# Kernel tuning notes

Measured on AMD Instinct MI355X. Metric: run time of the kernel, lower is better.

## Reference

```python
import jax, jax.numpy as jnp
import numpy as np

H_IMG = W_IMG = 1024
H_MAP = W_MAP = 64
SCALE = 16  # img // fmap, both axes
SCALES = [2, 2.5, 3, 3.5, 4, 5]
RATIOS = [0.5, 1.5, 2.0, 2.5, 3, 3.5, 4]
A = len(SCALES) * len(RATIOS)  # 42
POS_T, NEG_T = 0.5, 0.3


def _anchors_np():
    # generate_base_anchors + generate_anchor_boxes (down_h = down_w = SCALE)
    base = np.zeros((A, 4), np.float32)
    cy = cx = SCALE / 2.0
    i = 0
    for s in SCALES:
        for ar in RATIOS:
            h = SCALE * s * np.sqrt(ar)
            w = SCALE * s * np.sqrt(1.0 / ar)
            base[i] = [cy - h / 2.0, cx - w / 2.0, cy + h / 2.0, cx + w / 2.0]
            i += 1
    sy = np.arange(H_MAP) * SCALE
    sx = np.arange(W_MAP) * SCALE
    gx, gy = np.meshgrid(sx, sy)
    shifts = np.stack([gy.ravel(), gx.ravel(), gy.ravel(), gx.ravel()], axis=1)
    # order (H, W, A) -> matches conf.permute(0,2,3,1) flatten
    return (base[None, :, :] + shifts[:, None, :]).reshape(-1, 4).astype(np.float32)


def _conv(x, w, b):
    y = jax.lax.conv_general_dilated(x, w, (1, 1), 'SAME',
                                     dimension_numbers=('NCHW', 'OIHW', 'NCHW'))
    return y + b[None, :, None, None]


def setup_inputs() -> dict:
    key = jax.random.key(0)
    ks = jax.random.split(key, 10)
    B, N, C, Hm, Wm, HID = 8, 20, 256, 64, 64, 512
    feature_map = jax.random.normal(ks[0], (B, C, Hm, Wm), dtype=jnp.float32)
    # valid GT boxes in pixel xyxy-style (d0<d2, d1<d3), last 5 per image padded -1
    p0 = jax.random.uniform(ks[1], (B, N)) * 860.0
    p1 = jax.random.uniform(ks[2], (B, N)) * 860.0
    s0 = jax.random.uniform(ks[3], (B, N)) * 144.0 + 16.0
    s1 = jax.random.uniform(ks[4], (B, N)) * 144.0 + 16.0
    gt_bboxes = jnp.stack([p0, p1, p0 + s0, p1 + s1], axis=-1)
    gt_bboxes = gt_bboxes.at[:, 15:, :].set(-1.0)
    gt_classes = jax.random.randint(ks[5], (B, N), 0, 10)
    conv1_w = jax.random.normal(ks[6], (HID, C, 3, 3), dtype=jnp.float32) * 0.02
    conv1_b = jnp.zeros((HID,), jnp.float32)
    conf_w = jax.random.normal(ks[7], (A, HID, 1, 1), dtype=jnp.float32) * 0.02
    conf_b = jnp.zeros((A,), jnp.float32)
    reg_w = jax.random.normal(ks[8], (4 * A, HID, 1, 1), dtype=jnp.float32) * 0.02
    reg_b = jnp.zeros((4 * A,), jnp.float32)
    return {"feature_map": feature_map, "gt_bboxes": gt_bboxes, "gt_classes": gt_classes,
            "conv1_w": conv1_w, "conv1_b": conv1_b, "conf_w": conf_w, "conf_b": conf_b,
            "reg_w": reg_w, "reg_b": reg_b}


def reference(feature_map, gt_bboxes, gt_classes, conv1_w, conv1_b,
              conf_w, conf_b, reg_w, reg_b):
    anc = jnp.asarray(_anchors_np())           # [M,4]
    B = feature_map.shape[0]
    M = anc.shape[0]                           # H*W*A

    # project_bboxes p2a: divide by scale, keep -1 padding
    pad = gt_bboxes == -1.0
    g = jnp.where(pad, -1.0, gt_bboxes / float(SCALE))  # [B,N,4]
    valid = g[..., 0] >= 0                                # [B,N]
    g_safe = jnp.where(valid[..., None], g, jnp.array([0.0, 0.0, 1.0, 1.0]))

    # pairwise IoU [B,M,N] (vectorized get_iou_mat; invalid GT -> 0)
    tl = jnp.maximum(anc[None, :, None, :2], g_safe[:, None, :, :2])
    br = jnp.minimum(anc[None, :, None, 2:], g_safe[:, None, :, 2:])
    wh = jnp.clip(br - tl, 0.0)
    inter = wh[..., 0] * wh[..., 1]
    area_a = (anc[:, 2] - anc[:, 0]) * (anc[:, 3] - anc[:, 1])
    area_g = (g_safe[..., 2] - g_safe[..., 0]) * (g_safe[..., 3] - g_safe[..., 1])
    iou = inter / (area_a[None, :, None] + area_g[:, None, :] - inter)
    iou = jnp.where(valid[:, None, :], iou, 0.0)

    # positive assignment: per-GT argmax anchors + IoU > pos_thresh
    max_per_gt = iou.max(axis=1, keepdims=True)            # [B,1,N]
    pos_mask = ((iou == max_per_gt) & (max_per_gt > 0)) | (iou > POS_T)
    pos_any = pos_mask.any(axis=-1)                        # [B,M]
    a2g = jnp.argmax(iou, axis=2)                          # [B,M]
    max_per_anc = iou.max(axis=2)                          # [B,M]

    gt_for_anc = jnp.take_along_axis(g_safe, a2g[:, :, None], axis=1)  # [B,M,4]
    anc_b = jnp.broadcast_to(anc, (B, M, 4))
    gt_sel = jnp.where(pos_any[..., None], gt_for_anc, anc_b)  # safe for log

    # calc_gt_offsets (cxcywh encode), computed for all anchors, masked later
    a_c = (anc_b[..., :2] + anc_b[..., 2:]) * 0.5
    a_s = anc_b[..., 2:] - anc_b[..., :2]
    g_c = (gt_sel[..., :2] + gt_sel[..., 2:]) * 0.5
    g_s = gt_sel[..., 2:] - gt_sel[..., :2]
    off_gt = jnp.concatenate([(g_c - a_c) / a_s, jnp.log(g_s / a_s)], axis=-1)
    off_gt = off_gt.reshape(-1, 4)                          # [B*M,4]

    # ProposalModule head (dropout is a no-op in eval)
    x = jax.nn.relu(_conv(feature_map, conv1_w, conv1_b))
    conf = _conv(x, conf_w, conf_b)                         # [B,A,H,W]
    reg = _conv(x, reg_w, reg_b)                            # [B,4A,H,W]
    cflat = conf.transpose(0, 2, 3, 1).reshape(-1)          # [B*M]
    offp = reg.transpose(0, 2, 3, 1).reshape(-1, 4)         # [B*M,4]

    pf = pos_any.reshape(-1).astype(jnp.float32)
    P = pf.sum()

    # cls loss: BCE-with-logits, label 1 on positives, 0 on P sampled negatives
    cls_pos = (jax.nn.softplus(-cflat) * pf).sum() / P
    neg = max_per_anc.reshape(-1) < NEG_T
    scores = jax.random.uniform(jax.random.key(7), cflat.shape)
    scores = jnp.where(neg, scores, 2.0)
    ranks = jnp.argsort(jnp.argsort(scores))               # random sample = rank < P
    sel = (neg & (ranks < P)).astype(jnp.float32)
    cls_neg = (jax.nn.softplus(cflat) * sel).sum() / sel.sum()
    cls_loss = 0.5 * (cls_pos + cls_neg)

    d = offp - off_gt
    ad = jnp.abs(d)
    sl1 = jnp.where(ad < 1.0, 0.5 * ad * ad, ad - 0.5)
    reg_loss = (sl1 * pf[:, None]).sum() / (P * 4.0)

    return cls_loss + reg_loss
```

## Files before the change

kernel.cpp:

```cpp
#include <hip/hip_runtime.h>
#include <hip/hip_fp16.h>
#include <stdint.h>

constexpr int B_  = 8, HM = 64, WM = 64, A_ = 42, CIN = 256, HIDN = 512;
constexpr int M_  = HM * WM * A_;
constexpr int NA  = B_ * M_;
constexpr int HALF = NA / 2;
constexpr int KK  = CIN * 9;
constexpr float POS_T = 0.5f;

constexpr int WINY = 10, WINX = 10, WPIX = WINY * WINX;
constexpr int PERIMG = A_ * WPIX;
constexpr int WBLK = (PERIMG + 511) / 512;
constexpr int NMAXB = WBLK * B_;

constexpr int MAXPOS = 4096, MAXSEL = 4096, MAXCAND = 16384, MAXTIE = 256;
constexpr int MAXPIX = 1024;
constexpr uint32_t VCAND = 16384u;

constexpr int KSPL = 8, KCH = KK / KSPL;
constexpr int NSTRIP = MAXPIX / 64;
constexpr int NOCH = 4;
constexpr int NTILE = NSTRIP * NOCH * KSPL;
constexpr int TFBLK = HALF / 512;
constexpr int WCVTB = (HIDN * KK / 4) / 512;
constexpr int NBLK_TF = NMAXB + TFBLK + WCVTB;

constexpr size_t OFF_CTRL  = 0;
constexpr size_t OFF_BINS  = 256;
constexpr size_t OFF_MAXGT = 768;
constexpr size_t OFF_SLOT  = 2048;
constexpr size_t MS_END    = 133120;
constexpr size_t OFF_PLIST = 133120;
constexpr size_t OFF_POSL  = 137216;
constexpr size_t OFF_SELL  = 153600;
constexpr size_t OFF_CAND  = 169984;
constexpr size_t OFF_PART  = 301056;
constexpr size_t OFF_APATCH= 8689664;
constexpr size_t OFF_WF16  = 13408256;
constexpr size_t OFF_HFIN  = 15767552;


__device__ __forceinline__ unsigned short f2bf(float f) {
  uint32_t x = __float_as_uint(f);
  uint32_t r = x + 0x7FFFu + ((x >> 16) & 1u);
  return (unsigned short)(r >> 16);
}
__device__ __forceinline__ float bf2f(unsigned short h) {
  return __uint_as_float(((uint32_t)h) << 16);
}
__device__ __forceinline__ uint32_t f2h2(float a, float b) {
  return (uint32_t)__half_as_ushort(__float2half_rn(a)) |
         ((uint32_t)__half_as_ushort(__float2half_rn(b)) << 16);
}

typedef _Float16 h8v __attribute__((ext_vector_type(8)));
typedef float f4v __attribute__((ext_vector_type(4)));

__device__ __forceinline__ float iou_pair(float ay0, float ax0, float ay1, float ax1,
                                          float areaA, float g0, float g1, float g2, float g3,
                                          float areaG) {
#pragma clang fp contract(off)
  float ty = fmaxf(ay0, g0), tx = fmaxf(ax0, g1);
  float by = fminf(ay1, g2), bx = fminf(ax1, g3);
  float hy = by - ty; hy = fmaxf(hy, 0.f);
  float hx = bx - tx; hx = fmaxf(hx, 0.f);
  float inter = hy * hx;
  return inter / (areaA + areaG - inter);
}

__device__ __forceinline__ void anchor_box(const float* basef, int a, int y, int x,
                                           float& ay0, float& ax0, float& ay1, float& ax1,
                                           float& areaA) {
#pragma clang fp contract(off)
  double sy = 16.0 * (double)y, sx = 16.0 * (double)x;
  ay0 = (float)((double)basef[a * 4 + 0] + sy);
  ax0 = (float)((double)basef[a * 4 + 1] + sx);
  ay1 = (float)((double)basef[a * 4 + 2] + sy);
  ax1 = (float)((double)basef[a * 4 + 3] + sx);
  areaA = (ay1 - ay0) * (ax1 - ax0);
}

__device__ __forceinline__ void fill_base(float* sbase, int t) {
  if (t < 42) {
    const double SC[6] = {2.0, 2.5, 3.0, 3.5, 4.0, 5.0};
    const double RA[7] = {0.5, 1.5, 2.0, 2.5, 3.0, 3.5, 4.0};
    int si = t / 7, ri = t - si * 7;
    double h = 16.0 * SC[si] * sqrt(RA[ri]);
    double w = 16.0 * SC[si] * sqrt(1.0 / RA[ri]);
    sbase[t * 4 + 0] = (float)(8.0 - h / 2.0);
    sbase[t * 4 + 1] = (float)(8.0 - w / 2.0);
    sbase[t * 4 + 2] = (float)(8.0 + h / 2.0);
    sbase[t * 4 + 3] = (float)(8.0 + w / 2.0);
  }
}

__device__ __forceinline__ void fill_gt(const float* gt, int b, float* sg, float* sarea,
                                        unsigned* sval, int t) {
  if (t < 20) {
#pragma clang fp contract(off)
    float g4[4];
    for (int d = 0; d < 4; d++) {
      float v = gt[(b * 20 + t) * 4 + d];
      g4[d] = (v == -1.0f) ? -1.0f : v * 0.0625f;
    }
    unsigned valid = (g4[0] >= 0.0f) ? 1u : 0u;
    if (!valid) { g4[0] = 0.f; g4[1] = 0.f; g4[2] = 1.f; g4[3] = 1.f; }
    sg[t * 4 + 0] = g4[0]; sg[t * 4 + 1] = g4[1]; sg[t * 4 + 2] = g4[2]; sg[t * 4 + 3] = g4[3];
    sarea[t] = (g4[2] - g4[0]) * (g4[3] - g4[1]);
    sval[t] = valid;
  }
}

__device__ __forceinline__ void claim_pixel(char* ws, int pixg) {
  int* slotmap = (int*)(ws + OFF_SLOT);
  if (atomicCAS((unsigned*)&slotmap[pixg], 0u, 0xFFFFFFFFu) == 0u) {
    unsigned s = atomicAdd((unsigned*)(ws + OFF_CTRL) + 2, 1u);
    if (s < MAXPIX) { ((int*)(ws + OFF_PLIST))[s] = pixg; slotmap[pixg] = (int)s + 1; }
    else slotmap[pixg] = -1;
  }
}

__device__ __forceinline__ float softplusf(float x) {
  return fmaxf(x, 0.f) + log1pf(expf(-fabsf(x)));
}
__device__ __forceinline__ float sl1(float d) {
  float ad = fabsf(d);
  return ad < 1.f ? 0.5f * ad * ad : ad - 0.5f;
}

__device__ __forceinline__ void tf_round(uint32_t& x0, uint32_t& x1, int r) {
  x0 += x1; x1 = (x1 << r) | (x1 >> (32 - r)); x1 ^= x0;
}
__device__ __forceinline__ void threefry(uint32_t c0, uint32_t c1, uint32_t& o0, uint32_t& o1) {
  const uint32_t k0 = 0u, k1 = 7u;
  const uint32_t k2 = k0 ^ k1 ^ 0x1BD11BDAu;
  uint32_t x0 = c0 + k0, x1 = c1 + k1;
  tf_round(x0, x1, 13); tf_round(x0, x1, 15); tf_round(x0, x1, 26); tf_round(x0, x1, 6);
  x0 += k1; x1 += k2 + 1u;
  tf_round(x0, x1, 17); tf_round(x0, x1, 29); tf_round(x0, x1, 16); tf_round(x0, x1, 24);
  x0 += k2; x1 += k0 + 2u;
  tf_round(x0, x1, 13); tf_round(x0, x1, 15); tf_round(x0, x1, 26); tf_round(x0, x1, 6);
  x0 += k0; x1 += k1 + 3u;
  tf_round(x0, x1, 17); tf_round(x0, x1, 29); tf_round(x0, x1, 16); tf_round(x0, x1, 24);
  x0 += k1; x1 += k2 + 4u;
  tf_round(x0, x1, 13); tf_round(x0, x1, 15); tf_round(x0, x1, 26); tf_round(x0, x1, 6);
  x0 += k2; x1 += k0 + 5u;
  o0 = x0; o1 = x1;
}

__device__ __forceinline__ void dev_threefry_emit(char* ws, int p, int lane) {
  uint32_t o0, o1; threefry((uint32_t)p, (uint32_t)(p + HALF), o0, o1);
  uint32_t v0 = o0 >> 9, v1 = o1 >> 9;
  unsigned* ctrl = (unsigned*)(ws + OFF_CTRL);
  unsigned* bins = (unsigned*)(ws + OFF_BINS);
  uint2* cand = (uint2*)(ws + OFF_CAND);
  bool h0 = v0 < VCAND, h1 = v1 < VCAND;
  unsigned long long m0 = __ballot(h0), m1 = __ballot(h1);
  if (m0 | m1) {
    int n0 = __popcll(m0);
    int leader = (int)__ffsll(m0 | m1) - 1;
    unsigned base = 0;
    if (lane == leader) base = atomicAdd(&ctrl[3], (unsigned)(n0 + __popcll(m1)));
    base = (unsigned)__shfl((int)base, leader, 64);
    unsigned long long below = (1ull << lane) - 1ull;
    if (h0) {
      unsigned s = base + (unsigned)__popcll(m0 & below);
      if (s < MAXCAND) cand[s] = make_uint2(v0, (unsigned)p);
      atomicAdd(&bins[v0 >> 7], 1u);
    }
    if (h1) {
      unsigned s = base + (unsigned)n0 + (unsigned)__popcll(m1 & below);
      if (s < MAXCAND) cand[s] = make_uint2(v1, (unsigned)(p + HALF));
      atomicAdd(&bins[v1 >> 7], 1u);
    }
  }
}

__global__ void __launch_bounds__(512) kTF(const float* __restrict__ gt,
                                           const float* __restrict__ w1, char* ws) {
  __shared__ float sbase[168], sg[80], sarea[20];
  __shared__ unsigned sval[20];
  __shared__ int smax[20];
  int t = threadIdx.x, lane = t & 63;
  if (blockIdx.x < NMAXB) {
    int b = blockIdx.x / WBLK, blk = blockIdx.x - b * WBLK;
    fill_base(sbase, t);
    fill_gt(gt, b, sg, sarea, sval, t);
    if (t < 20) smax[t] = 0;
    __syncthreads();
    int idx = blk * 512 + t;
    bool ok = idx < PERIMG;
    float ay0 = 0.f, ax0 = 0.f, ay1 = 0.f, ax1 = 0.f, areaA = 1.f;
    if (ok) {
      int a = idx / WPIX, pp = idx - a * WPIX;
      int y = pp / WINX, x = pp - y * WINX;
      anchor_box(sbase, a, y, x, ay0, ax0, ay1, ax1, areaA);
    }
#pragma unroll
    for (int n = 0; n < 20; n++) {
      float io = 0.f;
      if (ok && sval[n]) io = iou_pair(ay0, ax0, ay1, ax1, areaA,
                                       sg[n * 4], sg[n * 4 + 1], sg[n * 4 + 2],
                                       sg[n * 4 + 3], sarea[n]);
#pragma unroll
      for (int off = 32; off >= 1; off >>= 1) io = fmaxf(io, __shfl_xor(io, off, 64));
      if ((t & 63) == 0 && io > 0.f) atomicMax(&smax[n], __float_as_int(io));
    }
    __syncthreads();
    if (t < 20 && smax[t] != 0)
      atomicMax((int*)(ws + OFF_MAXGT) + b * 20 + t, smax[t]);
  } else if (blockIdx.x < NMAXB + TFBLK) {
    int p = ((int)blockIdx.x - NMAXB) * 512 + t;
    if (p < HALF) dev_threefry_emit(ws, p, lane);
  } else {
    int q = ((int)blockIdx.x - (NMAXB + TFBLK)) * 512 + t;
    float4 v = ((const float4*)w1)[q];
    uint2 o;
    o.x = f2h2(v.x, v.y);
    o.y = f2h2(v.z, v.w);
    ((uint2*)(ws + OFF_WF16))[q] = o;
  }
}

__global__ void __launch_bounds__(512) kPos2(const float* __restrict__ gt, char* ws) {
  __shared__ float sbase[168], sg[80], sarea[20], smg[20];
  __shared__ unsigned sval[20];
  int b = blockIdx.y, t = threadIdx.x;
  unsigned* ctrl = (unsigned*)(ws + OFF_CTRL);
  fill_base(sbase, t);
  fill_gt(gt, b, sg, sarea, sval, t);
  if (t < 20) smg[t] = __int_as_float(((int*)(ws + OFF_MAXGT))[b * 20 + t]);
  __syncthreads();
  int idx = blockIdx.x * 512 + t;
  bool pos = false;
  unsigned packv = 0;
  int pixg = 0;
  if (idx < PERIMG) {
    int a = idx / WPIX, pp = idx - a * WPIX;
    int y = pp / WINX, x = pp - y * WINX;
    float ay0, ax0, ay1, ax1, areaA;
    anchor_box(sbase, a, y, x, ay0, ax0, ay1, ax1, areaA);
    float best = -1.f; int arg = 0;
#pragma unroll
    for (int n = 0; n < 20; n++) {
      float io = 0.f;
      if (sval[n]) io = iou_pair(ay0, ax0, ay1, ax1, areaA,
                                 sg[n * 4], sg[n * 4 + 1], sg[n * 4 + 2],
                                 sg[n * 4 + 3], sarea[n]);
      if (io > best) { best = io; arg = n; }
      float mg = smg[n];
      pos = pos || ((io == mg) && (mg > 0.f)) || (io > POS_T);
    }
    if (pos) {
      int pix = y * 64 + x;
      int i = b * M_ + pix * 42 + a;
      packv = (unsigned)i | ((unsigned)arg << 21);
      pixg = b * 4096 + pix;
    }
  }
  unsigned long long mask = __ballot(pos);
  if (mask) {
    int lane = t & 63;
    int leader = (int)__ffsll(mask) - 1;
    unsigned base = 0;
    if (lane == leader) base = atomicAdd(&ctrl[0], (unsigned)__popcll(mask));
    base = (unsigned)__shfl((int)base, leader, 64);
    if (pos) {
      unsigned slot = base + (unsigned)__popcll(mask & ((1ull << lane) - 1ull));
      if (slot < MAXPOS) ((unsigned*)(ws + OFF_POSL))[slot] = packv;
      claim_pixel(ws, pixg);
    }
  }
}

__global__ void __launch_bounds__(1024) kSel(char* ws) {
  __shared__ unsigned selbins[128];
  __shared__ uint2 ties[MAXTIE];
  __shared__ unsigned tcnt, s_r, s_ucut;
  __shared__ int s_icut, s_cutbin;
  int t = threadIdx.x;
  unsigned* ctrl = (unsigned*)(ws + OFF_CTRL);
  const uint2* cand = (const uint2*)(ws + OFF_CAND);
  unsigned P = min(ctrl[0], (unsigned)MAXPOS);
  unsigned nc = min(ctrl[3], (unsigned)MAXCAND);
  if (t < 128) selbins[t] = ((const unsigned*)(ws + OFF_BINS))[t];
  if (t == 0) tcnt = 0;
  __syncthreads();
  if (t == 0) {
    unsigned cum = 0; int c = 0;
    for (; c < 128; c++) { if (cum + selbins[c] >= P) break; cum += selbins[c]; }
    if (c == 128) c = 127;
    s_cutbin = c; s_r = (P > cum) ? (P - cum) : 0u;
  }
  __syncthreads();
  int cutbin = s_cutbin;
  for (unsigned j = t; j < nc; j += 1024) {
    uint2 cj = cand[j];
    if ((int)(cj.x >> 7) == cutbin) {
      unsigned k = atomicAdd(&tcnt, 1u);
      if (k < MAXTIE) ties[k] = cj;
    }
  }
  __syncthreads();
  unsigned n = min(tcnt, (unsigned)MAXTIE);
  unsigned r = s_r; if (r > n) r = n;
  if (r == 0) {
    if (t == 0) { s_ucut = 0; s_icut = -1; }
  } else if (t < (int)n) {
    uint2 mine = ties[t];
    unsigned rank = 0;
    for (unsigned j = 0; j < n; j++) {
      uint2 o = ties[j];
      if (o.x < mine.x || (o.x == mine.x && (int)o.y < (int)mine.y)) rank++;
    }
    if (rank == r - 1) { s_ucut = mine.x; s_icut = (int)mine.y; }
  }
  __syncthreads();
  unsigned ucut = s_ucut; int icut = s_icut;
  unsigned total = (nc + 1023u) & ~1023u;
  for (unsigned j = t; j < total; j += 1024) {
    bool sel = false; uint2 cj = make_uint2(0u, 0u);
    if (j < nc) {
      cj = cand[j];
      sel = (cj.x < ucut) || (cj.x == ucut && (int)cj.y <= icut);
    }
    unsigned long long mask = __ballot(sel);
    if (mask) {
      int lane = t & 63;
      int leader = (int)__ffsll(mask) - 1;
      unsigned base = 0;
      if (lane == leader) base = atomicAdd(&ctrl[1], (unsigned)__popcll(mask));
      base = (unsigned)__shfl((int)base, leader, 64);
      if (sel) {
        unsigned slot = base + (unsigned)__popcll(mask & ((1ull << lane) - 1ull));
        if (slot < MAXSEL) {
          ((int*)(ws + OFF_SELL))[slot] = (int)cj.y;
          int bb = (int)cj.y / M_; int m = (int)cj.y - bb * M_;
          claim_pixel(ws, bb * 4096 + m / 42);
        }
      }
    }
  }
}

__global__ void __launch_bounds__(256) kIm2col(const float* __restrict__ fm, char* ws) {
  unsigned* ctrl = (unsigned*)(ws + OFF_CTRL);
  int npix = min((int)ctrl[2], MAXPIX);
  int blk = blockIdx.x;
  if (blk >= npix) return;
  int chunk = blockIdx.y;
  int pixg = ((const int*)(ws + OFF_PLIST))[blk];
  int b = pixg >> 12, pix = pixg & 4095;
  int y = pix >> 6, x = pix & 63;
  uint32_t* Ap = (uint32_t*)(ws + OFF_APATCH) + (size_t)blk * (KK / 2);
  int u0 = chunk * 384;
  for (int u = u0 + threadIdx.x; u < u0 + 384; u += 256) {
    float v[2];
#pragma unroll
    for (int h = 0; h < 2; h++) {
      int k = 2 * u + h;
      int ic = k / 9, r = k - ic * 9;
      int dy = r / 3, dx = r - dy * 3;
      int yy = y + dy - 1, xx = x + dx - 1;
      float vv = 0.f;
      if (yy >= 0 && yy < 64 && xx >= 0 && xx < 64)
        vv = fm[(((size_t)b * CIN + ic) * 64 + yy) * 64 + xx];
      v[h] = vv;
    }
    Ap[u] = f2h2(v[0], v[1]);
  }
}

__global__ void __launch_bounds__(256) kGemm(char* ws) {
  unsigned* ctrl = (unsigned*)(ws + OFF_CTRL);
  int npix = min((int)ctrl[2], MAXPIX);
  int tile = blockIdx.x;
  int strip = tile & 15, r2 = tile >> 4;
  int och = r2 & 3, ks = r2 >> 2;
  int px0 = strip * 64;
  if (px0 >= npix) return;
  int oc0 = och * 128, kb = ks * KCH;
  const _Float16* Ap = (const _Float16*)(ws + OFF_APATCH);
  const _Float16* Wf = (const _Float16*)(ws + OFF_WF16);
  int t = threadIdx.x, lane = t & 63, wv = t >> 6;
  int kq = lane >> 4;
  const _Float16* Arow = Ap + (size_t)(px0 + wv * 16 + (lane & 15)) * KK + kb + kq * 8;
  const _Float16* Wrow = Wf + (size_t)(oc0 + (lane & 15)) * KK + kb + kq * 8;
  f4v acc[8] = {};
#pragma unroll 3
  for (int s = 0; s < 9; s++) {
    h8v a = *(const h8v*)(Arow + s * 32);
#pragma unroll
    for (int o = 0; o < 8; o++) {
      h8v bfr = *(const h8v*)(Wrow + (size_t)o * 16 * KK + s * 32);
      acc[o] = __builtin_amdgcn_mfma_f32_16x16x32_f16(a, bfr, acc[o], 0, 0, 0);
    }
  }
  unsigned short* part = (unsigned short*)(ws + OFF_PART) + (size_t)ks * MAXPIX * HIDN;
  int colbase = oc0 + (lane & 15);
  int pxb = px0 + wv * 16 + kq * 4;
#pragma unroll
  for (int o = 0; o < 8; o++) {
#pragma unroll
    for (int r = 0; r < 4; r++) {
      int px = pxb + r;
      if (px < npix)
        part[(size_t)px * HIDN + colbase + o * 16] = f2bf(acc[o][r]);
    }
  }
}

__global__ void __launch_bounds__(256) kReduce(const float* __restrict__ b1, char* ws) {
  unsigned* ctrl = (unsigned*)(ws + OFF_CTRL);
  int npix = min((int)ctrl[2], MAXPIX);
  int px = blockIdx.x;
  if (px >= npix) return;
  int t = threadIdx.x;
  constexpr size_t PS = (size_t)MAXPIX * HIDN;
  const unsigned short* p0 = (const unsigned short*)(ws + OFF_PART);
  unsigned short* hf = (unsigned short*)(ws + OFF_HFIN);
  size_t off = (size_t)px * HIDN + t * 2;
  float s0 = b1[t * 2], s1 = b1[t * 2 + 1];
#pragma unroll
  for (int q = 0; q < KSPL; q++) {
    uint32_t v = *(const uint32_t*)(p0 + q * PS + off);
    s0 += bf2f((unsigned short)(v & 0xFFFFu));
    s1 += bf2f((unsigned short)(v >> 16));
  }
  s0 = fmaxf(s0, 0.f); s1 = fmaxf(s1, 0.f);
  *(uint32_t*)(hf + off) = f2h2(s0, s1);
}

__global__ void __launch_bounds__(256) kHead(const float* __restrict__ gt,
                                             const float* __restrict__ cw,
                                             const float* __restrict__ cb,
                                             const float* __restrict__ rw,
                                             const float* __restrict__ rb,
                                             char* ws, float* out) {
  __shared__ float sbase[168], sg[640];
  __shared__ float sacc[3];
  int t = threadIdx.x;
  fill_base(sbase, t);
  if (t < 160) {
#pragma clang fp contract(off)
    float g4[4];
    for (int d = 0; d < 4; d++) {
      float v = gt[t * 4 + d];
      g4[d] = (v == -1.0f) ? -1.0f : v * 0.0625f;
    }
    if (!(g4[0] >= 0.0f)) { g4[0] = 0.f; g4[1] = 0.f; g4[2] = 1.f; g4[3] = 1.f; }
    sg[t * 4 + 0] = g4[0]; sg[t * 4 + 1] = g4[1];
    sg[t * 4 + 2] = g4[2]; sg[t * 4 + 3] = g4[3];
  }
  if (t < 3) sacc[t] = 0.f;
  __syncthreads();
  unsigned* ctrl = (unsigned*)(ws + OFF_CTRL);
  float* accum = (float*)(ctrl + 16);
  int np = min((int)ctrl[0], MAXPOS);
  int ns = min((int)ctrl[1], MAXSEL);
  int nent = np + ns;
  const unsigned* posl = (const unsigned*)(ws + OFF_POSL);
  const int* sell = (const int*)(ws + OFF_SELL);
  const int* slotmap = (const int*)(ws + OFF_SLOT);
  const unsigned short* hfin = (const unsigned short*)(ws + OFF_HFIN);
  int lane = t & 63;
  int gwave = blockIdx.x * 4 + (t >> 6);
  int nwaves = gridDim.x * 4;
  for (int e = gwave; e < nent; e += nwaves) {
    bool isPos = e < np;
    int i, arg = 0;
    if (isPos) { unsigned pck = posl[e]; i = (int)(pck & 0x1FFFFFu); arg = (int)(pck >> 21); }
    else i = sell[e - np];
    int b = i / M_; int m = i - b * M_;
    int pix = m / 42; int a = m - pix * 42;
    int y = pix >> 6, x = pix & 63;
    int slot = slotmap[b * 4096 + pix] - 1;
    if (slot < 0 || slot >= MAXPIX) continue;
    float h[8];
    {
      h8v hv = *(const h8v*)(hfin + (size_t)slot * HIDN + lane * 8);
#pragma unroll
      for (int j = 0; j < 8; j++) h[j] = (float)hv[j];
    }
    const float* cwr = cw + (size_t)a * HIDN + lane * 8;
    float4 cA = *(const float4*)cwr;
    float4 cB = *(const float4*)(cwr + 4);
    float cp = h[0] * cA.x + h[1] * cA.y + h[2] * cA.z + h[3] * cA.w +
               h[4] * cB.x + h[5] * cB.y + h[6] * cB.z + h[7] * cB.w;
#pragma unroll
    for (int off = 32; off >= 1; off >>= 1) cp += __shfl_xor(cp, off, 64);
    float conf = cp + cb[a];
    if (isPos) {
      float rp[4];
#pragma unroll
      for (int d = 0; d < 4; d++) {
        const float* rwr = rw + (size_t)(a * 4 + d) * HIDN + lane * 8;
        float4 rA = *(const float4*)rwr;
        float4 rB = *(const float4*)(rwr + 4);
        float sd = h[0] * rA.x + h[1] * rA.y + h[2] * rA.z + h[3] * rA.w +
                   h[4] * rB.x + h[5] * rB.y + h[6] * rB.z + h[7] * rB.w;
#pragma unroll
        for (int off = 32; off >= 1; off >>= 1) sd += __shfl_xor(sd, off, 64);
        rp[d] = sd + rb[a * 4 + d];
      }
      if (lane == 0) {
#pragma clang fp contract(off)
        float ay0, ax0, ay1, ax1, areaA;
        anchor_box(sbase, a, y, x, ay0, ax0, ay1, ax1, areaA);
        const float* g = sg + (size_t)(b * 20 + arg) * 4;
        float acy = (ay0 + ay1) * 0.5f, acx = (ax0 + ax1) * 0.5f;
        float ah = ay1 - ay0, aw = ax1 - ax0;
        float gcy = (g[0] + g[2]) * 0.5f, gcx = (g[1] + g[3]) * 0.5f;
        float gh = g[2] - g[0], gw = g[3] - g[1];
        float t0 = (gcy - acy) / ah, t1 = (gcx - acx) / aw;
        float t2 = logf(gh / ah), t3 = logf(gw / aw);
        float sL = sl1(rp[0] - t0) + sl1(rp[1] - t1) + sl1(rp[2] - t2) + sl1(rp[3] - t3);
        atomicAdd(&sacc[2], sL);
        atomicAdd(&sacc[0], softplusf(-conf));
      }
    } else {
      if (lane == 0) atomicAdd(&sacc[1], softplusf(conf));
    }
  }
  __syncthreads();
  if (t == 0) {
    if (sacc[0] != 0.f) atomicAdd(&accum[0], sacc[0]);
    if (sacc[1] != 0.f) atomicAdd(&accum[1], sacc[1]);
    if (sacc[2] != 0.f) atomicAdd(&accum[2], sacc[2]);
    __threadfence();
    unsigned done = atomicAdd(&ctrl[10], 1u);
    if (done == gridDim.x - 1) {
      __threadfence();
      float P = (float)min((int)ctrl[0], MAXPOS);
      float S = (float)min((int)ctrl[1], MAXSEL);
      float cls = 0.5f * (accum[0] / P + accum[1] / S);
      out[0] = cls + accum[2] / (P * 4.0f);
    }
  }
}

extern "C" void kernel_launch(void* const* d_in, const int* in_sizes, int n_in,
                              void* d_out, int out_size, void* d_ws, size_t ws_size,
                              hipStream_t stream) {
  const float* fm = (const float*)d_in[0];
  const float* gt = (const float*)d_in[1];
  const float* w1 = (const float*)d_in[3];
  const float* b1 = (const float*)d_in[4];
  const float* cw = (const float*)d_in[5];
  const float* cb = (const float*)d_in[6];
  const float* rw = (const float*)d_in[7];
  const float* rb = (const float*)d_in[8];
  char* ws = (char*)d_ws;
  float* out = (float*)d_out;

  hipMemsetAsync(ws, 0, MS_END, stream);
  kTF<<<NBLK_TF, 512, 0, stream>>>(gt, w1, ws);
  kPos2<<<dim3(WBLK, B_), 512, 0, stream>>>(gt, ws);
  kSel<<<1, 1024, 0, stream>>>(ws);
  kIm2col<<<dim3(MAXPIX, 3), 256, 0, stream>>>(fm, ws);
  kGemm<<<NTILE, 256, 0, stream>>>(ws);
  kReduce<<<MAXPIX, 256, 0, stream>>>(b1, ws);
  kHead<<<256, 256, 0, stream>>>(gt, cw, cb, rw, rb, ws, out);
}
```

Baseline: 177.8 us.

## Fold selection into last kPos2 block and fuse split-K reduce into GEMM

The separate single-block kSel kernel is removed. Its work now runs in the last kPos2 block to finish, detected with an atomic ticket counter, which saves one launch. The GEMM changes from a split-K grid that wrote bf16 partials to global memory plus a separate kReduce kernel. Now each block handles 16 pixels and its 8 waves split K, reducing through shared memory with bias, ReLU and fp16 store fused in. This drops the partial-sum round trip and a launch, but gives fewer pixels per block and adds relaxed-atomic completion logic in kHead.

```diff
diff --git a/kernel.cpp b/kernel.cpp
--- a/kernel.cpp
+++ b/kernel.cpp
@@ -18,10 +18,7 @@
 constexpr int MAXPIX = 1024;
 constexpr uint32_t VCAND = 16384u;
 
-constexpr int KSPL = 8, KCH = KK / KSPL;
-constexpr int NSTRIP = MAXPIX / 64;
-constexpr int NOCH = 4;
-constexpr int NTILE = NSTRIP * NOCH * KSPL;
+constexpr int KCH = 288;
 constexpr int TFBLK = HALF / 512;
 constexpr int WCVTB = (HIDN * KK / 4) / 512;
 constexpr int NBLK_TF = NMAXB + TFBLK + WCVTB;
@@ -35,7 +32,6 @@
 constexpr size_t OFF_POSL  = 137216;
 constexpr size_t OFF_SELL  = 153600;
 constexpr size_t OFF_CAND  = 169984;
-constexpr size_t OFF_PART  = 301056;
 constexpr size_t OFF_APATCH= 8689664;
 constexpr size_t OFF_WF16  = 13408256;
 constexpr size_t OFF_HFIN  = 15767552;
@@ -226,7 +222,11 @@
 __global__ void __launch_bounds__(512) kPos2(const float* __restrict__ gt, char* ws) {
   __shared__ float sbase[168], sg[80], sarea[20], smg[20];
   __shared__ unsigned sval[20];
-  int b = blockIdx.y, t = threadIdx.x;
+  __shared__ unsigned selbins[128];
+  __shared__ uint2 ties[MAXTIE];
+  __shared__ unsigned tcnt, s_r, s_ucut;
+  __shared__ int s_icut, s_cutbin, s_last;
+  int b = blockIdx.y, t = threadIdx.x, lane = t & 63;
   unsigned* ctrl = (unsigned*)(ws + OFF_CTRL);
   fill_base(sbase, t);
   fill_gt(gt, b, sg, sarea, sval, t);
@@ -261,7 +261,6 @@
   }
   unsigned long long mask = __ballot(pos);
   if (mask) {
-    int lane = t & 63;
     int leader = (int)__ffsll(mask) - 1;
     unsigned base = 0;
     if (lane == leader) base = atomicAdd(&ctrl[0], (unsigned)__popcll(mask));
@@ -272,18 +271,19 @@
       claim_pixel(ws, pixg);
     }
   }
-}
-
-__global__ void __launch_bounds__(1024) kSel(char* ws) {
-  __shared__ unsigned selbins[128];
-  __shared__ uint2 ties[MAXTIE];
-  __shared__ unsigned tcnt, s_r, s_ucut;
-  __shared__ int s_icut, s_cutbin;
-  int t = threadIdx.x;
-  unsigned* ctrl = (unsigned*)(ws + OFF_CTRL);
+  __syncthreads();
+  if (t == 0) {
+    unsigned r = __hip_atomic_fetch_add(&ctrl[11], 1u, __ATOMIC_RELAXED,
+                                        __HIP_MEMORY_SCOPE_AGENT);
+    s_last = (r == (unsigned)(WBLK * B_) - 1) ? 1 : 0;
+  }
+  __syncthreads();
+  if (!s_last) return;
   const uint2* cand = (const uint2*)(ws + OFF_CAND);
-  unsigned P = min(ctrl[0], (unsigned)MAXPOS);
-  unsigned nc = min(ctrl[3], (unsigned)MAXCAND);
+  unsigned P = min(__hip_atomic_load(&ctrl[0], __ATOMIC_RELAXED,
+                                     __HIP_MEMORY_SCOPE_AGENT), (unsigned)MAXPOS);
+  unsigned nc = min(__hip_atomic_load(&ctrl[3], __ATOMIC_RELAXED,
+                                      __HIP_MEMORY_SCOPE_AGENT), (unsigned)MAXCAND);
   if (t < 128) selbins[t] = ((const unsigned*)(ws + OFF_BINS))[t];
   if (t == 0) tcnt = 0;
   __syncthreads();
@@ -295,7 +295,7 @@
   }
   __syncthreads();
   int cutbin = s_cutbin;
-  for (unsigned j = t; j < nc; j += 1024) {
+  for (unsigned j = t; j < nc; j += 512) {
     uint2 cj = cand[j];
     if ((int)(cj.x >> 7) == cutbin) {
       unsigned k = atomicAdd(&tcnt, 1u);
@@ -318,22 +318,21 @@
   }
   __syncthreads();
   unsigned ucut = s_ucut; int icut = s_icut;
-  unsigned total = (nc + 1023u) & ~1023u;
-  for (unsigned j = t; j < total; j += 1024) {
+  unsigned total = (nc + 511u) & ~511u;
+  for (unsigned j = t; j < total; j += 512) {
     bool sel = false; uint2 cj = make_uint2(0u, 0u);
     if (j < nc) {
       cj = cand[j];
       sel = (cj.x < ucut) || (cj.x == ucut && (int)cj.y <= icut);
     }
-    unsigned long long mask = __ballot(sel);
-    if (mask) {
-      int lane = t & 63;
-      int leader = (int)__ffsll(mask) - 1;
+    unsigned long long m2 = __ballot(sel);
+    if (m2) {
+      int leader = (int)__ffsll(m2) - 1;
       unsigned base = 0;
-      if (lane == leader) base = atomicAdd(&ctrl[1], (unsigned)__popcll(mask));
+      if (lane == leader) base = atomicAdd(&ctrl[1], (unsigned)__popcll(m2));
       base = (unsigned)__shfl((int)base, leader, 64);
       if (sel) {
-        unsigned slot = base + (unsigned)__popcll(mask & ((1ull << lane) - 1ull));
+        unsigned slot = base + (unsigned)__popcll(m2 & ((1ull << lane) - 1ull));
         if (slot < MAXSEL) {
           ((int*)(ws + OFF_SELL))[slot] = (int)cj.y;
           int bb = (int)cj.y / M_; int m = (int)cj.y - bb * M_;
@@ -372,20 +371,20 @@
   }
 }
 
-__global__ void __launch_bounds__(256) kGemm(char* ws) {
+__global__ void __launch_bounds__(512) kGemm(const float* __restrict__ b1, char* ws) {
+  __shared__ float red[8][16][132];
   unsigned* ctrl = (unsigned*)(ws + OFF_CTRL);
   int npix = min((int)ctrl[2], MAXPIX);
-  int tile = blockIdx.x;
-  int strip = tile & 15, r2 = tile >> 4;
-  int och = r2 & 3, ks = r2 >> 2;
-  int px0 = strip * 64;
+  int strip = blockIdx.x, och = blockIdx.y;
+  int px0 = strip * 16;
   if (px0 >= npix) return;
-  int oc0 = och * 128, kb = ks * KCH;
+  int oc0 = och * 128;
   const _Float16* Ap = (const _Float16*)(ws + OFF_APATCH);
   const _Float16* Wf = (const _Float16*)(ws + OFF_WF16);
   int t = threadIdx.x, lane = t & 63, wv = t >> 6;
   int kq = lane >> 4;
-  const _Float16* Arow = Ap + (size_t)(px0 + wv * 16 + (lane & 15)) * KK + kb + kq * 8;
+  int kb = wv * KCH;
+  const _Float16* Arow = Ap + (size_t)(px0 + (lane & 15)) * KK + kb + kq * 8;
   const _Float16* Wrow = Wf + (size_t)(oc0 + (lane & 15)) * KK + kb + kq * 8;
   f4v acc[8] = {};
 #pragma unroll 3
@@ -397,39 +396,31 @@
       acc[o] = __builtin_amdgcn_mfma_f32_16x16x32_f16(a, bfr, acc[o], 0, 0, 0);
     }
   }
-  unsigned short* part = (unsigned short*)(ws + OFF_PART) + (size_t)ks * MAXPIX * HIDN;
-  int colbase = oc0 + (lane & 15);
-  int pxb = px0 + wv * 16 + kq * 4;
 #pragma unroll
   for (int o = 0; o < 8; o++) {
-#pragma unroll
-    for (int r = 0; r < 4; r++) {
-      int px = pxb + r;
-      if (px < npix)
-        part[(size_t)px * HIDN + colbase + o * 16] = f2bf(acc[o][r]);
-    }
-  }
-}
-
-__global__ void __launch_bounds__(256) kReduce(const float* __restrict__ b1, char* ws) {
-  unsigned* ctrl = (unsigned*)(ws + OFF_CTRL);
-  int npix = min((int)ctrl[2], MAXPIX);
-  int px = blockIdx.x;
-  if (px >= npix) return;
-  int t = threadIdx.x;
-  constexpr size_t PS = (size_t)MAXPIX * HIDN;
-  const unsigned short* p0 = (const unsigned short*)(ws + OFF_PART);
-  unsigned short* hf = (unsigned short*)(ws + OFF_HFIN);
-  size_t off = (size_t)px * HIDN + t * 2;
-  float s0 = b1[t * 2], s1 = b1[t * 2 + 1];
-#pragma unroll
-  for (int q = 0; q < KSPL; q++) {
-    uint32_t v = *(const uint32_t*)(p0 + q * PS + off);
-    s0 += bf2f((unsigned short)(v & 0xFFFFu));
-    s1 += bf2f((unsigned short)(v >> 16));
-  }
-  s0 = fmaxf(s0, 0.f); s1 = fmaxf(s1, 0.f);
-  *(uint32_t*)(hf + off) = f2h2(s0, s1);
+    int col = o * 16 + (lane & 15);
+#pragma unroll
+    for (int r = 0; r < 4; r++)
+      red[wv][kq * 4 + r][col] = acc[o][r];
+  }
+  __syncthreads();
+  int row = t >> 5, colg = t & 31;
+  if (px0 + row < npix) {
+    float s4[4];
+#pragma unroll
+    for (int j = 0; j < 4; j++) s4[j] = b1[oc0 + colg * 4 + j];
+#pragma unroll
+    for (int w = 0; w < 8; w++)
+#pragma unroll
+      for (int j = 0; j < 4; j++) s4[j] += red[w][row][colg * 4 + j];
+#pragma unroll
+    for (int j = 0; j < 4; j++) s4[j] = fmaxf(s4[j], 0.f);
+    unsigned short* hf = (unsigned short*)(ws + OFF_HFIN);
+    uint2 o2;
+    o2.x = f2h2(s4[0], s4[1]);
+    o2.y = f2h2(s4[2], s4[3]);
+    *(uint2*)(hf + (size_t)(px0 + row) * HIDN + oc0 + colg * 4) = o2;
+  }
 }
 
 __global__ void __launch_bounds__(256) kHead(const float* __restrict__ gt,
@@ -528,14 +519,17 @@
     if (sacc[0] != 0.f) atomicAdd(&accum[0], sacc[0]);
     if (sacc[1] != 0.f) atomicAdd(&accum[1], sacc[1]);
     if (sacc[2] != 0.f) atomicAdd(&accum[2], sacc[2]);
-    __threadfence();
-    unsigned done = atomicAdd(&ctrl[10], 1u);
+    asm volatile("s_waitcnt vmcnt(0)" ::: "memory");
+    unsigned done = __hip_atomic_fetch_add(&ctrl[10], 1u, __ATOMIC_RELAXED,
+                                           __HIP_MEMORY_SCOPE_AGENT);
     if (done == gridDim.x - 1) {
-      __threadfence();
+      float a0 = __hip_atomic_load(&accum[0], __ATOMIC_RELAXED, __HIP_MEMORY_SCOPE_AGENT);
+      float a1 = __hip_atomic_load(&accum[1], __ATOMIC_RELAXED, __HIP_MEMORY_SCOPE_AGENT);
+      float a2 = __hip_atomic_load(&accum[2], __ATOMIC_RELAXED, __HIP_MEMORY_SCOPE_AGENT);
       float P = (float)min((int)ctrl[0], MAXPOS);
       float S = (float)min((int)ctrl[1], MAXSEL);
-      float cls = 0.5f * (accum[0] / P + accum[1] / S);
-      out[0] = cls + accum[2] / (P * 4.0f);
+      float cls = 0.5f * (a0 / P + a1 / S);
+      out[0] = cls + a2 / (P * 4.0f);
     }
   }
 }
@@ -557,9 +551,7 @@
   hipMemsetAsync(ws, 0, MS_END, stream);
   kTF<<<NBLK_TF, 512, 0, stream>>>(gt, w1, ws);
   kPos2<<<dim3(WBLK, B_), 512, 0, stream>>>(gt, ws);
-  kSel<<<1, 1024, 0, stream>>>(ws);
   kIm2col<<<dim3(MAXPIX, 3), 256, 0, stream>>>(fm, ws);
-  kGemm<<<NTILE, 256, 0, stream>>>(ws);
-  kReduce<<<MAXPIX, 256, 0, stream>>>(b1, ws);
+  kGemm<<<dim3(MAXPIX / 16, 4), 512, 0, stream>>>(b1, ws);
   kHead<<<256, 256, 0, stream>>>(gt, cw, cb, rw, rb, ws, out);
 }
```

After: 180.0 us. Within noise of the previous version (+1.2%).
